# Kernel optimization log

Hardware: AMD Instinct MI355X
Metric: run time of the kernel (lower is better)

The kernel has to match this reference:

```python
import jax, jax.numpy as jnp
import numpy as np

DEPTH = 6
B, D, E, H = 8192, 256, 256, 50
N_INNER = (1 << (DEPTH - 1)) - 1   # 31
N_LEAF = 1 << (DEPTH - 1)          # 32


def setup_inputs() -> dict:
    key = jax.random.key(0)
    ks = jax.random.split(key, 16)
    g = lambda k, shape, fan: (jax.random.normal(k, shape, dtype=jnp.float32)
                               / jnp.sqrt(jnp.float32(fan)))
    return {
        "x": jax.random.normal(ks[0], (B, D), dtype=jnp.float32),
        "enc_W": g(ks[1], (4, E, E), E),
        "enc_b": jnp.zeros((4, E), jnp.float32),
        # inner nodes, stacked over N_INNER
        "in_W1": g(ks[2], (N_INNER, E, H), E),
        "in_b1": jnp.zeros((N_INNER, H), jnp.float32),
        "in_Ww": g(ks[3], (N_INNER, H, D), H),
        "in_bw": jnp.zeros((N_INNER, D), jnp.float32),
        "in_Wb": g(ks[4], (N_INNER, H), H),
        "in_bb": jnp.zeros((N_INNER,), jnp.float32),
        "in_Wbeta": g(ks[5], (N_INNER, H), H),
        "in_bbeta": jnp.zeros((N_INNER,), jnp.float32),
        # leaf models, stacked over N_LEAF
        "lf_W1": g(ks[6], (N_LEAF, E, E), E),
        "lf_b1": jnp.zeros((N_LEAF, E), jnp.float32),
        "lf_W2": g(ks[7], (N_LEAF, E), E),
        "lf_b2": jnp.zeros((N_LEAF,), jnp.float32),
    }


def reference(x, enc_W, enc_b, in_W1, in_b1, in_Ww, in_bw, in_Wb, in_bb,
              in_Wbeta, in_bbeta, lf_W1, lf_b1, lf_W2, lf_b2):
    batch = x.shape[0]
    # encoder: 4 relu Dense layers
    emb = x
    for i in range(4):
        emb = jax.nn.relu(emb @ enc_W[i] + enc_b[i])

    # all inner-node gates in one batched pass  -> pR: [N_INNER, B]
    h = jax.nn.relu(jnp.einsum('be,neh->nbh', emb, in_W1) + in_b1[:, None, :])
    w = jax.nn.softmax(jnp.einsum('nbh,nhd->nbd', h, in_Ww) + in_bw[:, None, :], axis=-1)
    b = jnp.einsum('nbh,nh->nb', h, in_Wb) + in_bb[:, None]
    beta = jnp.einsum('nbh,nh->nb', h, in_Wbeta) + in_bbeta[:, None]
    pR = jax.nn.sigmoid(beta * (jnp.einsum('nbd,bd->nb', w, x) + b))

    # all leaf MLPs in one batched pass  -> y_leaf: [N_LEAF, B]
    hl = jax.nn.relu(jnp.einsum('be,leh->lbh', emb, lf_W1) + lf_b1[:, None, :])
    y_leaf = jnp.einsum('lbh,lh->lb', hl, lf_W2) + lf_b2[:, None]

    # path probabilities (heap ordering; right child weighted by pR)
    prob = jnp.ones((batch, 1), dtype=x.dtype)
    idx = 0
    for level in range(DEPTH - 1):
        cnt = 1 << level
        p = pR[idx:idx + cnt].T                       # [B, cnt]
        prob = jnp.stack([prob * (1.0 - p), prob * p], axis=-1).reshape(batch, 2 * cnt)
        idx += cnt

    return jnp.sum(prob * y_leaf.T, axis=1, keepdims=True)  # [B, 1]
```

## Files before the change

kernel.cpp:

```cpp
#include <hip/hip_runtime.h>


#define B_ROWS 8192
#define HDIM 50
#define HPAD 64

typedef _Float16 f16;
typedef _Float16 f16x8 __attribute__((ext_vector_type(8)));
typedef _Float16 f16x4 __attribute__((ext_vector_type(4)));
typedef float f32x4 __attribute__((ext_vector_type(4)));

static __device__ __forceinline__ f32x4 mfma16(f16x8 a, f16x8 b, f32x4 c) {
  return __builtin_amdgcn_mfma_f32_16x16x32_f16(a, b, c, 0, 0, 0);
}

static __device__ __forceinline__ void gload16(const void* g, void* l) {
  __builtin_amdgcn_global_load_lds(
      (const __attribute__((address_space(1))) unsigned int*)g,
      (__attribute__((address_space(3))) unsigned int*)l, 16, 0, 0);
}

__global__ void k_cast_f16(const float* __restrict__ in, f16* __restrict__ out, int n4) {
  int i = blockIdx.x * blockDim.x + threadIdx.x;
  if (i < n4) {
    float4 v = reinterpret_cast<const float4*>(in)[i];
    f16x4 o = { (f16)v.x, (f16)v.y, (f16)v.z, (f16)v.w };
    reinterpret_cast<f16x4*>(out)[i] = o;
  }
}

__global__ void k_tcast(const float* __restrict__ in, f16* __restrict__ out,
                        int R, int C, int Rp, int Cp) {
  __shared__ float t[32][33];
  const int s = blockIdx.z;
  const int r0 = blockIdx.x * 32, c0 = blockIdx.y * 32;
  const int tx = threadIdx.x, ty = threadIdx.y;
  const float* ip = in + (size_t)s * R * C;
  f16* op = out + (size_t)s * Cp * Rp;
#pragma unroll
  for (int i = 0; i < 4; ++i) {
    int r = r0 + ty + 8 * i, c = c0 + tx;
    t[ty + 8 * i][tx] = (r < R && c < C) ? ip[(size_t)r * C + c] : 0.f;
  }
  __syncthreads();
#pragma unroll
  for (int i = 0; i < 4; ++i) {
    int c = c0 + ty + 8 * i, r = r0 + tx;
    if (c < Cp && r < Rp) op[(size_t)c * Rp + r] = (f16)t[tx][ty + 8 * i];
  }
}

__global__ void k_prep_ww(const float* __restrict__ Ww, const float* __restrict__ Wb,
                          const float* __restrict__ Wbeta, f16* __restrict__ WwE) {
  const int node = blockIdx.x;
  const int d = threadIdx.x;
  f16 row[64];
#pragma unroll
  for (int h = 0; h < 64; ++h)
    row[h] = (h < HDIM) ? (f16)Ww[((size_t)node * HDIM + h) * 256 + d] : (f16)0.f;
  f16* dst = WwE + (size_t)node * 272 * 64 + (size_t)d * 64;
#pragma unroll
  for (int j = 0; j < 8; ++j) *(f16x8*)&dst[j * 8] = *(const f16x8*)&row[j * 8];
  if (d < 16) {
    f16 er[64];
#pragma unroll
    for (int h = 0; h < 64; ++h) {
      float v = 0.f;
      if (d == 0 && h < HDIM) v = Wb[node * HDIM + h];
      if (d == 1 && h < HDIM) v = Wbeta[node * HDIM + h];
      er[h] = (f16)v;
    }
    f16* dst2 = WwE + (size_t)node * 272 * 64 + (size_t)(256 + d) * 64;
#pragma unroll
    for (int j = 0; j < 8; ++j) *(f16x8*)&dst2[j * 8] = *(const f16x8*)&er[j * 8];
  }
}

__global__ __launch_bounds__(256) void k_enc4(const float* __restrict__ x,
    const f16* __restrict__ encWT, const float* __restrict__ enc_b,
    f16* __restrict__ emb) {
  __shared__ f16 act[2][32][264];
  __shared__ f16 Bt[256][72];
  const int tid = threadIdx.x;
  const int wave = tid >> 6, lane = tid & 63;
  const int grp = lane >> 4, lid = lane & 15;
  const int row0 = blockIdx.x * 32;
  const int sr = tid >> 3, sc = (tid & 7) * 8;

  {
    const int xr = tid >> 3, xc = (tid & 7) * 32;
    const float* src = x + (size_t)(row0 + xr) * 256 + xc;
#pragma unroll
    for (int j = 0; j < 4; ++j) {
      float4 a = ((const float4*)src)[2 * j];
      float4 b = ((const float4*)src)[2 * j + 1];
      f16x8 o = { (f16)a.x, (f16)a.y, (f16)a.z, (f16)a.w,
                  (f16)b.x, (f16)b.y, (f16)b.z, (f16)b.w };
      *(f16x8*)&act[0][xr][xc + 8 * j] = o;
    }
  }
  __syncthreads();

  for (int l = 0; l < 4; ++l) {
    const int cur = l & 1, nxt = cur ^ 1;
    f32x4 acc[2][4] = {};
    for (int kt = 0; kt < 4; ++kt) {
#pragma unroll
      for (int p = 0; p < 8; ++p)
        *(f16x8*)&Bt[p * 32 + sr][sc] =
            *(const f16x8*)&encWT[(size_t)l * 65536 + (size_t)(p * 32 + sr) * 256 + kt * 64 + sc];
      __syncthreads();
#pragma unroll
      for (int kk = 0; kk < 2; ++kk) {
        f16x8 af[2], bf[4];
#pragma unroll
        for (int m = 0; m < 2; ++m)
          af[m] = *(const f16x8*)&act[cur][m * 16 + lid][kt * 64 + kk * 32 + grp * 8];
#pragma unroll
        for (int n = 0; n < 4; ++n)
          bf[n] = *(const f16x8*)&Bt[wave * 64 + n * 16 + lid][kk * 32 + grp * 8];
#pragma unroll
        for (int m = 0; m < 2; ++m)
#pragma unroll
          for (int n = 0; n < 4; ++n) acc[m][n] = mfma16(af[m], bf[n], acc[m][n]);
      }
      __syncthreads();
    }
#pragma unroll
    for (int n = 0; n < 4; ++n) {
      const int col = wave * 64 + n * 16 + lid;
      const float bv = enc_b[l * 256 + col];
#pragma unroll
      for (int m = 0; m < 2; ++m)
#pragma unroll
        for (int r = 0; r < 4; ++r) {
          float v = acc[m][n][r] + bv;
          act[nxt][m * 16 + grp * 4 + r][col] = (f16)(v > 0.f ? v : 0.f);
        }
    }
    __syncthreads();
  }
  {
    const int xr = tid >> 3, xc = (tid & 7) * 32;
#pragma unroll
    for (int j = 0; j < 4; ++j)
      *(f16x8*)&emb[(size_t)(row0 + xr) * 256 + xc + 8 * j] =
          *(const f16x8*)&act[0][xr][xc + 8 * j];
  }
}

__global__ __launch_bounds__(256, 2) void k_inner(const f16* __restrict__ emb,
    const f16* __restrict__ W1T_all, const float* __restrict__ b1_all,
    const f16* __restrict__ WwE_all, const f16* __restrict__ x_h,
    const float* __restrict__ bw_all, const float* __restrict__ bb_all,
    const float* __restrict__ bbeta_all, float* __restrict__ pR) {
  __shared__ f16 et[64][264];
  __shared__ f16 hbuf[4][64][72];

  const int tid = threadIdx.x;
  const int wave = tid >> 6, lane = tid & 63;
  const int grp = lane >> 4, lid = lane & 15;
  const int row0 = blockIdx.x * 64;
  const int node_raw = blockIdx.y * 4 + wave;
  const int node = node_raw < 31 ? node_raw : 30;

  {
    const int r = tid >> 2, cb = (tid & 3) * 64;
#pragma unroll
    for (int j = 0; j < 8; ++j)
      *(f16x8*)&et[r][cb + 8 * j] =
          *(const f16x8*)&emb[(size_t)(row0 + r) * 256 + cb + 8 * j];
  }
  __syncthreads();

  const f16* W1T = W1T_all + (size_t)node * HPAD * 256;
  const f16* WwE = WwE_all + (size_t)node * 272 * 64;

  f32x4 acc1[4][4] = {};
  f16x8 wf[2][4];
#pragma unroll
  for (int h4 = 0; h4 < 4; ++h4)
    wf[0][h4] = *(const f16x8*)&W1T[(size_t)(h4 * 16 + lid) * 256 + grp * 8];
  for (int kt = 0; kt < 8; ++kt) {
    const int cur = kt & 1, nxt = cur ^ 1;
    if (kt < 7) {
#pragma unroll
      for (int h4 = 0; h4 < 4; ++h4)
        wf[nxt][h4] = *(const f16x8*)&W1T[(size_t)(h4 * 16 + lid) * 256 +
                                          (kt + 1) * 32 + grp * 8];
    }
    f16x8 af[4];
#pragma unroll
    for (int m = 0; m < 4; ++m)
      af[m] = *(const f16x8*)&et[m * 16 + lid][kt * 32 + grp * 8];
#pragma unroll
    for (int h4 = 0; h4 < 4; ++h4)
#pragma unroll
      for (int m = 0; m < 4; ++m)
        acc1[h4][m] = mfma16(wf[cur][h4], af[m], acc1[h4][m]);
  }
#pragma unroll
  for (int h4 = 0; h4 < 4; ++h4) {
    const int hc = h4 * 16 + grp * 4;
    float bva[4];
#pragma unroll
    for (int r = 0; r < 4; ++r)
      bva[r] = (hc + r < HDIM) ? b1_all[node * HDIM + hc + r] : 0.f;
#pragma unroll
    for (int m = 0; m < 4; ++m) {
      f16x4 hv;
#pragma unroll
      for (int r = 0; r < 4; ++r) {
        float v = acc1[h4][m][r] + bva[r];
        hv[r] = (f16)(v > 0.f ? v : 0.f);
      }
      *(f16x4*)&hbuf[wave][m * 16 + lid][hc] = hv;
    }
  }
  __syncthreads();
  {
    const int r = tid >> 2, cb = (tid & 3) * 64;
#pragma unroll
    for (int j = 0; j < 8; ++j)
      *(f16x8*)&et[r][cb + 8 * j] =
          *(const f16x8*)&x_h[(size_t)(row0 + r) * 256 + cb + 8 * j];
  }
  __syncthreads();

  f32x4 accm[4] = {};
#pragma unroll
  for (int kk = 0; kk < 2; ++kk) {
    f16x8 wmini = *(const f16x8*)&WwE[(size_t)(256 + lid) * 64 + kk * 32 + grp * 8];
#pragma unroll
    for (int m = 0; m < 4; ++m) {
      f16x8 hf = *(const f16x8*)&hbuf[wave][m * 16 + lid][kk * 32 + grp * 8];
      accm[m] = mfma16(wmini, hf, accm[m]);
    }
  }

  float s[4] = {0.f, 0.f, 0.f, 0.f}, dt[4] = {0.f, 0.f, 0.f, 0.f};
  for (int c = 0; c < 4; ++c) {
    f16x8 awf[2][4];
#pragma unroll
    for (int kk = 0; kk < 2; ++kk)
#pragma unroll
      for (int n4 = 0; n4 < 4; ++n4)
        awf[kk][n4] = *(const f16x8*)&WwE[(size_t)(c * 64 + n4 * 16 + lid) * 64 +
                                          kk * 32 + grp * 8];
    f32x4 acc2[4][4] = {};
#pragma unroll
    for (int kk = 0; kk < 2; ++kk) {
      f16x8 hf[4];
#pragma unroll
      for (int m = 0; m < 4; ++m)
        hf[m] = *(const f16x8*)&hbuf[wave][m * 16 + lid][kk * 32 + grp * 8];
#pragma unroll
      for (int n4 = 0; n4 < 4; ++n4)
#pragma unroll
        for (int m = 0; m < 4; ++m)
          acc2[n4][m] = mfma16(awf[kk][n4], hf[m], acc2[n4][m]);
    }
#pragma unroll
    for (int n4 = 0; n4 < 4; ++n4) {
      float4 bwv = *(const float4*)&bw_all[node * 256 + c * 64 + n4 * 16 + grp * 4];
      float bwa[4] = {bwv.x, bwv.y, bwv.z, bwv.w};
#pragma unroll
      for (int m = 0; m < 4; ++m) {
        f16x4 xv = *(const f16x4*)&et[m * 16 + lid][c * 64 + n4 * 16 + grp * 4];
#pragma unroll
        for (int r = 0; r < 4; ++r) {
          float e = __expf(acc2[n4][m][r] + bwa[r]);
          s[m] += e;
          dt[m] += e * (float)xv[r];
        }
      }
    }
  }
#pragma unroll
  for (int m = 0; m < 4; ++m) {
    s[m]  += __shfl_xor(s[m], 16, 64);  s[m]  += __shfl_xor(s[m], 32, 64);
    dt[m] += __shfl_xor(dt[m], 16, 64); dt[m] += __shfl_xor(dt[m], 32, 64);
  }
  if (grp == 0 && node_raw < 31) {
    const float bbv = bb_all[node], bbetav = bbeta_all[node];
#pragma unroll
    for (int m = 0; m < 4; ++m) {
      const int row = m * 16 + lid;
      float b = accm[m][0] + bbv;
      float beta = accm[m][1] + bbetav;
      float z = beta * (dt[m] / s[m] + b);
      pR[(size_t)(row0 + row) * 32 + node] = 1.f / (1.f + __expf(-z));
    }
  }
}

__global__ __launch_bounds__(512) void k_leaf(const f16* __restrict__ emb,
    const f16* __restrict__ W1T_all, const float* __restrict__ b1_all,
    const float* __restrict__ W2_all, const float* __restrict__ b2_all,
    float* __restrict__ y_leaf) {
  __shared__ f16 Albuf[2][256 * 64];
  __shared__ f16 Blbuf[2][256 * 64];
  __shared__ float red[4][256];
  const int tid = threadIdx.x;
  const int wave = tid >> 6, lane = tid & 63;
  const int wm = wave >> 2, wn = wave & 3;
  const int grp = lane >> 4, lid = lane & 15;
  const int row0 = blockIdx.x * 256;
  const int leaf = blockIdx.y;
  const f16* WT = W1T_all + (size_t)leaf * 65536;
  const float* b1 = b1_all + leaf * 256;
  const float* W2 = W2_all + leaf * 256;

  const int lrow = lane >> 3;
  const int sslot = (lane & 7) ^ lrow;
  const int swzA = (lid & 7);

#define LEAF_STAGE(buf, kt)                                                    \
  {                                                                            \
    _Pragma("unroll")                                                          \
    for (int r4 = 0; r4 < 4; ++r4) {                                           \
      const int rr = r4 * 64 + wave * 8 + lrow;                                \
      gload16(emb + (size_t)(row0 + rr) * 256 + (kt) * 64 + sslot * 8,         \
              (char*)&Albuf[buf][0] + r4 * 8192 + wave * 1024);                \
      gload16(WT + (size_t)rr * 256 + (kt) * 64 + sslot * 8,                   \
              (char*)&Blbuf[buf][0] + r4 * 8192 + wave * 1024);                \
    }                                                                          \
  }

  f32x4 acc[4][8] = {};
  LEAF_STAGE(0, 0);
  __syncthreads();
  for (int kt = 0; kt < 4; ++kt) {
    const int b = kt & 1;
    if (kt < 3) LEAF_STAGE(b ^ 1, kt + 1);
#pragma unroll
    for (int kk = 0; kk < 2; ++kk) {
      f16x8 af[8], bf[4];
#pragma unroll
      for (int rb = 0; rb < 8; ++rb) {
        const int row = wm * 128 + rb * 16 + lid;
        af[rb] = *(const f16x8*)((const char*)&Albuf[b][0] + row * 128 +
                                 (((kk * 4 + grp) ^ swzA) << 4));
      }
#pragma unroll
      for (int cb = 0; cb < 4; ++cb) {
        const int col = wn * 64 + cb * 16 + lid;
        bf[cb] = *(const f16x8*)((const char*)&Blbuf[b][0] + col * 128 +
                                 (((kk * 4 + grp) ^ swzA) << 4));
      }
#pragma unroll
      for (int cb = 0; cb < 4; ++cb)
#pragma unroll
        for (int rb = 0; rb < 8; ++rb)
          acc[cb][rb] = mfma16(bf[cb], af[rb], acc[cb][rb]);
    }
    if (kt < 3) __syncthreads();
  }
  float b1a[4][4], w2a[4][4];
#pragma unroll
  for (int cb = 0; cb < 4; ++cb) {
    float4 t1 = *(const float4*)&b1[wn * 64 + cb * 16 + grp * 4];
    float4 t2 = *(const float4*)&W2[wn * 64 + cb * 16 + grp * 4];
    b1a[cb][0] = t1.x; b1a[cb][1] = t1.y; b1a[cb][2] = t1.z; b1a[cb][3] = t1.w;
    w2a[cb][0] = t2.x; w2a[cb][1] = t2.y; w2a[cb][2] = t2.z; w2a[cb][3] = t2.w;
  }
  float rs[8] = {};
#pragma unroll
  for (int cb = 0; cb < 4; ++cb)
#pragma unroll
    for (int rb = 0; rb < 8; ++rb)
#pragma unroll
      for (int r = 0; r < 4; ++r) {
        float v = acc[cb][rb][r] + b1a[cb][r];
        v = v > 0.f ? v : 0.f;
        rs[rb] += v * w2a[cb][r];
      }
#pragma unroll
  for (int rb = 0; rb < 8; ++rb) {
    rs[rb] += __shfl_xor(rs[rb], 16, 64);
    rs[rb] += __shfl_xor(rs[rb], 32, 64);
  }
  __syncthreads();
  if (lane < 16)
#pragma unroll
    for (int rb = 0; rb < 8; ++rb)
      red[wn][wm * 128 + rb * 16 + lane] = rs[rb];
  __syncthreads();
  if (tid < 256) {
    float y = red[0][tid] + red[1][tid] + red[2][tid] + red[3][tid] + b2_all[leaf];
    y_leaf[(size_t)(row0 + tid) * 32 + leaf] = y;
  }
}

__global__ void k_combine(const float* __restrict__ pR, const float* __restrict__ y_leaf,
                          float* __restrict__ out) {
  const int b = blockIdx.x * 256 + threadIdx.x;
  float p[32], y[32];
  const float4* pp = (const float4*)(pR + (size_t)b * 32);
  const float4* yp = (const float4*)(y_leaf + (size_t)b * 32);
#pragma unroll
  for (int i = 0; i < 8; ++i) {
    float4 v = pp[i]; p[i*4] = v.x; p[i*4+1] = v.y; p[i*4+2] = v.z; p[i*4+3] = v.w;
    float4 w = yp[i]; y[i*4] = w.x; y[i*4+1] = w.y; y[i*4+2] = w.z; y[i*4+3] = w.w;
  }
  float o = 0.f;
#pragma unroll
  for (int l = 0; l < 32; ++l) {
    float pr = 1.f;
    int node = 0;
#pragma unroll
    for (int k = 0; k < 5; ++k) {
      const int bit = (l >> (4 - k)) & 1;
      const float pv = p[node];
      pr *= bit ? pv : (1.f - pv);
      node = 2 * node + 1 + bit;
    }
    o += pr * y[l];
  }
  out[b] = o;
}

extern "C" void kernel_launch(void* const* d_in, const int* in_sizes, int n_in,
                              void* d_out, int out_size, void* d_ws, size_t ws_size,
                              hipStream_t stream) {
  (void)in_sizes; (void)n_in; (void)out_size; (void)ws_size;
  const float* x        = (const float*)d_in[0];
  const float* enc_W    = (const float*)d_in[1];
  const float* enc_b    = (const float*)d_in[2];
  const float* in_W1    = (const float*)d_in[3];
  const float* in_b1    = (const float*)d_in[4];
  const float* in_Ww    = (const float*)d_in[5];
  const float* in_bw    = (const float*)d_in[6];
  const float* in_Wb    = (const float*)d_in[7];
  const float* in_bb    = (const float*)d_in[8];
  const float* in_Wbeta = (const float*)d_in[9];
  const float* in_bbeta = (const float*)d_in[10];
  const float* lf_W1    = (const float*)d_in[11];
  const float* lf_b1    = (const float*)d_in[12];
  const float* lf_W2    = (const float*)d_in[13];
  const float* lf_b2    = (const float*)d_in[14];
  float* out = (float*)d_out;

  char* ws = (char*)d_ws;
  f16* x_h     = (f16*)(ws);
  f16* emb     = (f16*)(ws + 4194304);
  f16* encWT   = (f16*)(ws + 8388608);
  f16* lfW1T   = (f16*)(ws + 8912896);
  f16* inW1T   = (f16*)(ws + 13107200);
  f16* WwE     = (f16*)(ws + 14123008);
  float* pR    = (float*)(ws + 15202304);
  float* y_leaf= (float*)(ws + 16250880);

  dim3 tb(32, 8);
  hipLaunchKernelGGL(k_cast_f16, dim3(2048), dim3(256), 0, stream, x, x_h, B_ROWS * 256 / 4);
  hipLaunchKernelGGL(k_tcast, dim3(8, 8, 4),  tb, 0, stream, enc_W, encWT, 256, 256, 256, 256);
  hipLaunchKernelGGL(k_tcast, dim3(8, 8, 32), tb, 0, stream, lf_W1, lfW1T, 256, 256, 256, 256);
  hipLaunchKernelGGL(k_tcast, dim3(8, 2, 31), tb, 0, stream, in_W1, inW1T, 256, 50, 256, 64);
  hipLaunchKernelGGL(k_prep_ww, dim3(31), dim3(256), 0, stream, in_Ww, in_Wb, in_Wbeta, WwE);

  hipLaunchKernelGGL(k_enc4, dim3(256), dim3(256), 0, stream, x, encWT, enc_b, emb);
  hipLaunchKernelGGL(k_inner, dim3(128, 8), dim3(256), 0, stream, emb, inW1T, in_b1,
                     WwE, x_h, in_bw, in_bb, in_bbeta, pR);
  hipLaunchKernelGGL(k_leaf, dim3(32, 32), dim3(512), 0, stream, emb, lfW1T, lf_b1, lf_W2, lf_b2, y_leaf);
  hipLaunchKernelGGL(k_combine, dim3(32), dim3(256), 0, stream, pR, y_leaf, out);
}
```

Baseline: 214.9 us.

## Merge prep kernels, pre-scale softmax by log2e, double-buffer Ww loads, swap grid order

Folds the five weight and input preparation launches into one k_prep kernel that dispatches on block index, which removes launch overhead. The Ww weights are pre-multiplied by log2(e) so the softmax can use exp2f. In k_inner the h fragments are hoisted out of the chunk loop and the Ww chunk loads are double-buffered by manual unrolling. The grid axes of k_inner and k_leaf are swapped so blocks sharing a row tile of emb run close together, which should improve cache reuse. Costs are higher register pressure, and the softmax logits now carry an extra fp16 rounding after the log2(e) scale.

```diff
diff --git a/kernel.cpp b/kernel.cpp
--- a/kernel.cpp
+++ b/kernel.cpp
@@ -4,6 +4,7 @@
 #define B_ROWS 8192
 #define HDIM 50
 #define HPAD 64
+#define LOG2E 1.44269504f
 
 typedef _Float16 f16;
 typedef _Float16 f16x8 __attribute__((ext_vector_type(8)));
@@ -20,59 +21,78 @@
       (__attribute__((address_space(3))) unsigned int*)l, 16, 0, 0);
 }
 
-__global__ void k_cast_f16(const float* __restrict__ in, f16* __restrict__ out, int n4) {
-  int i = blockIdx.x * blockDim.x + threadIdx.x;
-  if (i < n4) {
-    float4 v = reinterpret_cast<const float4*>(in)[i];
-    f16x4 o = { (f16)v.x, (f16)v.y, (f16)v.z, (f16)v.w };
-    reinterpret_cast<f16x4*>(out)[i] = o;
-  }
-}
-
-__global__ void k_tcast(const float* __restrict__ in, f16* __restrict__ out,
-                        int R, int C, int Rp, int Cp) {
-  __shared__ float t[32][33];
-  const int s = blockIdx.z;
-  const int r0 = blockIdx.x * 32, c0 = blockIdx.y * 32;
-  const int tx = threadIdx.x, ty = threadIdx.y;
-  const float* ip = in + (size_t)s * R * C;
-  f16* op = out + (size_t)s * Cp * Rp;
+static __device__ __forceinline__ void tcast_body(const float* ip, f16* op,
+    int R, int C, int Rp, int r0, int c0, int tx, int ty, float scale,
+    float t[32][33]) {
 #pragma unroll
   for (int i = 0; i < 4; ++i) {
     int r = r0 + ty + 8 * i, c = c0 + tx;
-    t[ty + 8 * i][tx] = (r < R && c < C) ? ip[(size_t)r * C + c] : 0.f;
+    t[ty + 8 * i][tx] = (r < R && c < C) ? ip[(size_t)r * C + c] * scale : 0.f;
   }
   __syncthreads();
 #pragma unroll
   for (int i = 0; i < 4; ++i) {
     int c = c0 + ty + 8 * i, r = r0 + tx;
-    if (c < Cp && r < Rp) op[(size_t)c * Rp + r] = (f16)t[tx][ty + 8 * i];
-  }
-}
-
-__global__ void k_prep_ww(const float* __restrict__ Ww, const float* __restrict__ Wb,
-                          const float* __restrict__ Wbeta, f16* __restrict__ WwE) {
-  const int node = blockIdx.x;
-  const int d = threadIdx.x;
-  f16 row[64];
-#pragma unroll
-  for (int h = 0; h < 64; ++h)
-    row[h] = (h < HDIM) ? (f16)Ww[((size_t)node * HDIM + h) * 256 + d] : (f16)0.f;
-  f16* dst = WwE + (size_t)node * 272 * 64 + (size_t)d * 64;
-#pragma unroll
-  for (int j = 0; j < 8; ++j) *(f16x8*)&dst[j * 8] = *(const f16x8*)&row[j * 8];
-  if (d < 16) {
-    f16 er[64];
-#pragma unroll
-    for (int h = 0; h < 64; ++h) {
-      float v = 0.f;
-      if (d == 0 && h < HDIM) v = Wb[node * HDIM + h];
-      if (d == 1 && h < HDIM) v = Wbeta[node * HDIM + h];
-      er[h] = (f16)v;
-    }
-    f16* dst2 = WwE + (size_t)node * 272 * 64 + (size_t)(256 + d) * 64;
-#pragma unroll
-    for (int j = 0; j < 8; ++j) *(f16x8*)&dst2[j * 8] = *(const f16x8*)&er[j * 8];
+    op[(size_t)c * Rp + r] = (f16)t[tx][ty + 8 * i];
+  }
+}
+
+__global__ __launch_bounds__(256) void k_prep(
+    const float* __restrict__ x, const float* __restrict__ enc_W,
+    const float* __restrict__ lf_W1, const float* __restrict__ in_W1,
+    const float* __restrict__ in_Ww, const float* __restrict__ in_Wb,
+    const float* __restrict__ in_Wbeta,
+    f16* __restrict__ x_h, f16* __restrict__ encWT, f16* __restrict__ lfW1T,
+    f16* __restrict__ inW1T, f16* __restrict__ WwE) {
+  __shared__ float t[32][33];
+  const int idx = blockIdx.x;
+  const int tid = threadIdx.x;
+  if (idx < 1024) {
+    const int e8 = idx * 256 + tid;
+    const float4* f4 = (const float4*)x;
+    float4 v0 = f4[e8 * 2], v1 = f4[e8 * 2 + 1];
+    f16x8 o = { (f16)v0.x, (f16)v0.y, (f16)v0.z, (f16)v0.w,
+                (f16)v1.x, (f16)v1.y, (f16)v1.z, (f16)v1.w };
+    ((f16x8*)x_h)[e8] = o;
+  } else if (idx < 3072) {
+    const int q = idx - 1024;
+    const int s = q >> 6, bx = (q & 63) >> 3, by = q & 7;
+    tcast_body(lf_W1 + (size_t)s * 65536, lfW1T + (size_t)s * 65536,
+               256, 256, 256, bx * 32, by * 32, tid & 31, tid >> 5, 1.f, t);
+  } else if (idx < 3328) {
+    const int q = idx - 3072;
+    const int s = q >> 6, bx = (q & 63) >> 3, by = q & 7;
+    tcast_body(enc_W + (size_t)s * 65536, encWT + (size_t)s * 65536,
+               256, 256, 256, bx * 32, by * 32, tid & 31, tid >> 5, 1.f, t);
+  } else if (idx < 3824) {
+    const int q = idx - 3328;
+    const int s = q >> 4, bx = (q & 15) >> 1, by = q & 1;
+    tcast_body(in_W1 + (size_t)s * 256 * HDIM, inW1T + (size_t)s * HPAD * 256,
+               256, HDIM, 256, bx * 32, by * 32, tid & 31, tid >> 5, 1.f, t);
+  } else {
+    const int node = idx - 3824;
+    const int d = tid;
+    f16 row[64];
+#pragma unroll
+    for (int h = 0; h < 64; ++h)
+      row[h] = (h < HDIM) ? (f16)(in_Ww[((size_t)node * HDIM + h) * 256 + d] * LOG2E)
+                          : (f16)0.f;
+    f16* dst = WwE + (size_t)node * 272 * 64 + (size_t)d * 64;
+#pragma unroll
+    for (int j = 0; j < 8; ++j) *(f16x8*)&dst[j * 8] = *(const f16x8*)&row[j * 8];
+    if (d < 16) {
+      f16 er[64];
+#pragma unroll
+      for (int h = 0; h < 64; ++h) {
+        float v = 0.f;
+        if (d == 0 && h < HDIM) v = in_Wb[node * HDIM + h];
+        if (d == 1 && h < HDIM) v = in_Wbeta[node * HDIM + h];
+        er[h] = (f16)v;
+      }
+      f16* dst2 = WwE + (size_t)node * 272 * 64 + (size_t)(256 + d) * 64;
+#pragma unroll
+      for (int j = 0; j < 8; ++j) *(f16x8*)&dst2[j * 8] = *(const f16x8*)&er[j * 8];
+    }
   }
 }
 
@@ -160,8 +180,8 @@
   const int tid = threadIdx.x;
   const int wave = tid >> 6, lane = tid & 63;
   const int grp = lane >> 4, lid = lane & 15;
-  const int row0 = blockIdx.x * 64;
-  const int node_raw = blockIdx.y * 4 + wave;
+  const int row0 = blockIdx.y * 64;
+  const int node_raw = blockIdx.x * 4 + wave;
   const int node = node_raw < 31 ? node_raw : 30;
 
   {
@@ -227,55 +247,72 @@
   }
   __syncthreads();
 
+  f16x8 hf[2][4];
+#pragma unroll
+  for (int kk = 0; kk < 2; ++kk)
+#pragma unroll
+    for (int m = 0; m < 4; ++m)
+      hf[kk][m] = *(const f16x8*)&hbuf[wave][m * 16 + lid][kk * 32 + grp * 8];
+
   f32x4 accm[4] = {};
-#pragma unroll
-  for (int kk = 0; kk < 2; ++kk) {
-    f16x8 wmini = *(const f16x8*)&WwE[(size_t)(256 + lid) * 64 + kk * 32 + grp * 8];
+  {
+    f16x8 wm0 = *(const f16x8*)&WwE[(size_t)(256 + lid) * 64 + grp * 8];
+    f16x8 wm1 = *(const f16x8*)&WwE[(size_t)(256 + lid) * 64 + 32 + grp * 8];
 #pragma unroll
     for (int m = 0; m < 4; ++m) {
-      f16x8 hf = *(const f16x8*)&hbuf[wave][m * 16 + lid][kk * 32 + grp * 8];
-      accm[m] = mfma16(wmini, hf, accm[m]);
-    }
+      accm[m] = mfma16(wm0, hf[0][m], accm[m]);
+      accm[m] = mfma16(wm1, hf[1][m], accm[m]);
+    }
+  }
+
+#define LOADW(buf, c)                                                          \
+  _Pragma("unroll")                                                            \
+  for (int kk = 0; kk < 2; ++kk)                                               \
+    _Pragma("unroll")                                                          \
+    for (int n4 = 0; n4 < 4; ++n4)                                             \
+      buf[kk][n4] = *(const f16x8*)&WwE[(size_t)((c) * 64 + n4 * 16 + lid) * 64 + \
+                                        kk * 32 + grp * 8];
+
+#define CHUNK(c, CUR)                                                          \
+  {                                                                            \
+    f32x4 acc2[4][4] = {};                                                     \
+    _Pragma("unroll")                                                          \
+    for (int kk = 0; kk < 2; ++kk)                                             \
+      _Pragma("unroll")                                                        \
+      for (int n4 = 0; n4 < 4; ++n4)                                           \
+        _Pragma("unroll")                                                      \
+        for (int m = 0; m < 4; ++m)                                            \
+          acc2[n4][m] = mfma16(CUR[kk][n4], hf[kk][m], acc2[n4][m]);           \
+    _Pragma("unroll")                                                          \
+    for (int n4 = 0; n4 < 4; ++n4) {                                           \
+      float4 bwv = *(const float4*)&bw_all[node * 256 + (c) * 64 + n4 * 16 + grp * 4]; \
+      float bwa[4] = {bwv.x * LOG2E, bwv.y * LOG2E, bwv.z * LOG2E, bwv.w * LOG2E}; \
+      _Pragma("unroll")                                                        \
+      for (int m = 0; m < 4; ++m) {                                            \
+        f16x4 xv = *(const f16x4*)&et[m * 16 + lid][(c) * 64 + n4 * 16 + grp * 4]; \
+        _Pragma("unroll")                                                      \
+        for (int r = 0; r < 4; ++r) {                                          \
+          float e = exp2f(acc2[n4][m][r] + bwa[r]);                            \
+          s[m] += e;                                                           \
+          dt[m] += e * (float)xv[r];                                           \
+        }                                                                      \
+      }                                                                        \
+    }                                                                          \
   }
 
   float s[4] = {0.f, 0.f, 0.f, 0.f}, dt[4] = {0.f, 0.f, 0.f, 0.f};
-  for (int c = 0; c < 4; ++c) {
-    f16x8 awf[2][4];
-#pragma unroll
-    for (int kk = 0; kk < 2; ++kk)
-#pragma unroll
-      for (int n4 = 0; n4 < 4; ++n4)
-        awf[kk][n4] = *(const f16x8*)&WwE[(size_t)(c * 64 + n4 * 16 + lid) * 64 +
-                                          kk * 32 + grp * 8];
-    f32x4 acc2[4][4] = {};
-#pragma unroll
-    for (int kk = 0; kk < 2; ++kk) {
-      f16x8 hf[4];
-#pragma unroll
-      for (int m = 0; m < 4; ++m)
-        hf[m] = *(const f16x8*)&hbuf[wave][m * 16 + lid][kk * 32 + grp * 8];
-#pragma unroll
-      for (int n4 = 0; n4 < 4; ++n4)
-#pragma unroll
-        for (int m = 0; m < 4; ++m)
-          acc2[n4][m] = mfma16(awf[kk][n4], hf[m], acc2[n4][m]);
-    }
-#pragma unroll
-    for (int n4 = 0; n4 < 4; ++n4) {
-      float4 bwv = *(const float4*)&bw_all[node * 256 + c * 64 + n4 * 16 + grp * 4];
-      float bwa[4] = {bwv.x, bwv.y, bwv.z, bwv.w};
-#pragma unroll
-      for (int m = 0; m < 4; ++m) {
-        f16x4 xv = *(const f16x4*)&et[m * 16 + lid][c * 64 + n4 * 16 + grp * 4];
-#pragma unroll
-        for (int r = 0; r < 4; ++r) {
-          float e = __expf(acc2[n4][m][r] + bwa[r]);
-          s[m] += e;
-          dt[m] += e * (float)xv[r];
-        }
-      }
-    }
-  }
+  f16x8 awfA[2][4], awfB[2][4];
+  LOADW(awfA, 0);
+  LOADW(awfB, 1);
+  CHUNK(0, awfA);
+  LOADW(awfA, 2);
+  CHUNK(1, awfB);
+  LOADW(awfB, 3);
+  CHUNK(2, awfA);
+  CHUNK(3, awfB);
+#undef LOADW
+#undef CHUNK
+
 #pragma unroll
   for (int m = 0; m < 4; ++m) {
     s[m]  += __shfl_xor(s[m], 16, 64);  s[m]  += __shfl_xor(s[m], 32, 64);
@@ -305,8 +342,8 @@
   const int wave = tid >> 6, lane = tid & 63;
   const int wm = wave >> 2, wn = wave & 3;
   const int grp = lane >> 4, lid = lane & 15;
-  const int row0 = blockIdx.x * 256;
-  const int leaf = blockIdx.y;
+  const int row0 = blockIdx.y * 256;
+  const int leaf = blockIdx.x;
   const f16* WT = W1T_all + (size_t)leaf * 65536;
   const float* b1 = b1_all + leaf * 256;
   const float* W2 = W2_all + leaf * 256;
@@ -356,6 +393,7 @@
     }
     if (kt < 3) __syncthreads();
   }
+#undef LEAF_STAGE
   float b1a[4][4], w2a[4][4];
 #pragma unroll
   for (int cb = 0; cb < 4; ++cb) {
@@ -451,15 +489,11 @@
   float* pR    = (float*)(ws + 15202304);
   float* y_leaf= (float*)(ws + 16250880);
 
-  dim3 tb(32, 8);
-  hipLaunchKernelGGL(k_cast_f16, dim3(2048), dim3(256), 0, stream, x, x_h, B_ROWS * 256 / 4);
-  hipLaunchKernelGGL(k_tcast, dim3(8, 8, 4),  tb, 0, stream, enc_W, encWT, 256, 256, 256, 256);
-  hipLaunchKernelGGL(k_tcast, dim3(8, 8, 32), tb, 0, stream, lf_W1, lfW1T, 256, 256, 256, 256);
-  hipLaunchKernelGGL(k_tcast, dim3(8, 2, 31), tb, 0, stream, in_W1, inW1T, 256, 50, 256, 64);
-  hipLaunchKernelGGL(k_prep_ww, dim3(31), dim3(256), 0, stream, in_Ww, in_Wb, in_Wbeta, WwE);
-
+  hipLaunchKernelGGL(k_prep, dim3(3855), dim3(256), 0, stream,
+                     x, enc_W, lf_W1, in_W1, in_Ww, in_Wb, in_Wbeta,
+                     x_h, encWT, lfW1T, inW1T, WwE);
   hipLaunchKernelGGL(k_enc4, dim3(256), dim3(256), 0, stream, x, encWT, enc_b, emb);
-  hipLaunchKernelGGL(k_inner, dim3(128, 8), dim3(256), 0, stream, emb, inW1T, in_b1,
+  hipLaunchKernelGGL(k_inner, dim3(8, 128), dim3(256), 0, stream, emb, inW1T, in_b1,
                      WwE, x_h, in_bw, in_bb, in_bbeta, pR);
   hipLaunchKernelGGL(k_leaf, dim3(32, 32), dim3(512), 0, stream, emb, lfW1T, lf_b1, lf_W2, lf_b2, y_leaf);
   hipLaunchKernelGGL(k_combine, dim3(32), dim3(256), 0, stream, pR, y_leaf, out);
```

New measurement: 211.0 us. No clear change (-1.8%).
